# Kernel tuning notes

Measured on AMD Instinct MI355X. Metric: run time of the kernel, lower is better.

Reference implementation:

```python
import jax, jax.numpy as jnp
import numpy as np

B, E, H, W = 32, 512, 16, 16
NH, HD = 8, 64          # num_heads = embed_dim // num_heads_channels, head_dim = 64
OUT = 512
S = H * W + 1           # spacial_dim**2 + 1 = 257 (mean token prepended)


def setup_inputs() -> dict:
    key = jax.random.key(0)
    ks = jax.random.split(key, 10)
    sc = 1.0 / np.sqrt(E).astype(np.float32)
    n = lambda k, sh, s=1.0: jax.random.normal(k, sh, jnp.float32) * s
    return {
        "x_real": n(ks[0], (B, E, H, W)),
        "x_imag": n(ks[1], (B, E, H, W)),
        # positional_embedding = (randn/sqrt(E)).to(complex64) -> imag part is zero
        "pos_r": n(ks[2], (E, S), sc),
        "pos_i": jnp.zeros((E, S), jnp.float32),
        # complex in-projection (packed q,k,v) and out-projection of the MHA
        "w_in_r": n(ks[3], (3 * E, E), sc),
        "w_in_i": n(ks[4], (3 * E, E), sc),
        "b_in_r": jnp.zeros((3 * E,), jnp.float32),
        "b_in_i": jnp.zeros((3 * E,), jnp.float32),
        "w_out_r": n(ks[5], (E, E), sc),
        "w_out_i": n(ks[6], (E, E), sc),
        "b_out_r": jnp.zeros((E,), jnp.float32),
        "b_out_i": jnp.zeros((E,), jnp.float32),
        # complex 1x1 conv projection == complex linear over channels
        "w_p_r": n(ks[7], (OUT, E), sc),
        "w_p_i": n(ks[8], (OUT, E), sc),
        "b_p_r": jnp.zeros((OUT,), jnp.float32),
        "b_p_i": jnp.zeros((OUT,), jnp.float32),
    }


def _attention_pool(x_real, x_imag, pos_r, pos_i, w_in_r, w_in_i, b_in_r, b_in_i,
                    w_out_r, w_out_i, b_out_r, b_out_i, w_p_r, w_p_i, b_p_r, b_p_i):
    cx = jax.lax.complex
    x = cx(x_real, x_imag).reshape(B, E, -1)                       # [b,c,HW]
    x = jnp.concatenate([x.mean(-1, keepdims=True), x], axis=-1)   # [b,c,S]
    x = x + cx(pos_r, pos_i)[None]                                 # + pos embed
    x = x.transpose(0, 2, 1)                                       # [b,S,E]

    qkv = jnp.einsum('bse,fe->bsf', x, cx(w_in_r, w_in_i)) + cx(b_in_r, b_in_i)
    q, k, v = jnp.split(qkv, 3, axis=-1)
    q = q.reshape(B, S, NH, HD) / jnp.sqrt(jnp.float32(HD))
    k = k.reshape(B, S, NH, HD)
    v = v.reshape(B, S, NH, HD)

    logits = jnp.einsum('bqhd,bkhd->bhqk', q, k)                   # complex scores
    # complex softmax handled separately on real/imag parts
    w = cx(jax.nn.softmax(logits.real, axis=-1),
           jax.nn.softmax(logits.imag, axis=-1))
    attn = jnp.einsum('bhqk,bkhd->bqhd', w, v).reshape(B, S, E)
    attn = jnp.einsum('bse,fe->bsf', attn, cx(w_out_r, w_out_i)) + cx(b_out_r, b_out_i)

    y = attn.transpose(0, 2, 1)                                    # [b,E,S]
    y = jnp.einsum('oc,bcs->bos', cx(w_p_r, w_p_i), y) + cx(b_p_r, b_p_i)[None, :, None]
    return y[:, :, 0]                                              # [b,OUT] complex64


def reference(x_real, x_imag, pos_r, pos_i, w_in_r, w_in_i, b_in_r, b_in_i,
              w_out_r, w_out_i, b_out_r, b_out_i, w_p_r, w_p_i, b_p_r, b_p_i):
    return _attention_pool(x_real, x_imag, pos_r, pos_i, w_in_r, w_in_i, b_in_r,
                           b_in_i, w_out_r, w_out_i, b_out_r, b_out_i,
                           w_p_r, w_p_i, b_p_r, b_p_i)
```

## Files before the change

### kernel.cpp

```cpp
#include <hip/hip_runtime.h>

#define B_  32
#define E_  512
#define HW_ 256
#define S_  257
#define NH_ 8
#define HD_ 64
#define EC_ 32
#define NCH_ (E_ / EC_)

__device__ __forceinline__ float wave_reduce(float v) {
  #pragma unroll
  for (int o = 32; o > 0; o >>= 1) v += __shfl_down(v, o, 64);
  return v;
}

__global__ void k_mean(const float* __restrict__ xr, const float* __restrict__ xi,
                       const float* __restrict__ pos_r, const float* __restrict__ pos_i,
                       float* __restrict__ mr, float* __restrict__ mi) {
  int wid  = (blockIdx.x * blockDim.x + threadIdx.x) >> 6;
  int lane = threadIdx.x & 63;
  int e = wid & (E_ - 1);
  const float* pr = xr + (size_t)wid * HW_;
  const float* pi = xi + (size_t)wid * HW_;
  float sr = 0.f, si = 0.f;
  #pragma unroll
  for (int j = 0; j < HW_; j += 64) { sr += pr[j + lane]; si += pi[j + lane]; }
  sr = wave_reduce(sr); si = wave_reduce(si);
  if (lane == 0) {
    mr[wid] = sr * (1.f / HW_) + pos_r[(size_t)e * S_];
    mi[wid] = si * (1.f / HW_) + pos_i[(size_t)e * S_];
  }
}

__global__ void k_q0(const float* __restrict__ mr, const float* __restrict__ mi,
                     const float* __restrict__ w_in_r, const float* __restrict__ w_in_i,
                     const float* __restrict__ b_in_r, const float* __restrict__ b_in_i,
                     float* __restrict__ q0r, float* __restrict__ q0i) {
  int wid  = (blockIdx.x * blockDim.x + threadIdx.x) >> 6;
  int lane = threadIdx.x & 63;
  int b = wid >> 9, f = wid & (E_ - 1);
  const float* wr = w_in_r + (size_t)f * E_;
  const float* wi = w_in_i + (size_t)f * E_;
  float ar = 0.f, ai = 0.f;
  #pragma unroll
  for (int e = lane; e < E_; e += 64) {
    float Xr = mr[b * E_ + e];
    float Xi = mi[b * E_ + e];
    float Cr = wr[e], Ci = wi[e];
    ar += Xr * Cr - Xi * Ci;
    ai += Xr * Ci + Xi * Cr;
  }
  ar = wave_reduce(ar); ai = wave_reduce(ai);
  if (lane == 0) {
    q0r[wid] = (ar + b_in_r[f]) * 0.125f;
    q0i[wid] = (ai + b_in_i[f]) * 0.125f;
  }
}

__global__ void k_u(const float* __restrict__ q0r, const float* __restrict__ q0i,
                    const float* __restrict__ w_in_r, const float* __restrict__ w_in_i,
                    float* __restrict__ ur, float* __restrict__ ui) {
  int bh = blockIdx.x;
  int b = bh >> 3, h = bh & 7;
  int e = threadIdx.x;
  __shared__ float qr[HD_], qi[HD_];
  if (threadIdx.x < HD_) {
    qr[threadIdx.x] = q0r[b * E_ + h * HD_ + threadIdx.x];
    qi[threadIdx.x] = q0i[b * E_ + h * HD_ + threadIdx.x];
  }
  __syncthreads();
  float ar = 0.f, ai = 0.f;
  #pragma unroll 8
  for (int d = 0; d < HD_; ++d) {
    float Wr = w_in_r[(size_t)(E_ + h * HD_ + d) * E_ + e];
    float Wi = w_in_i[(size_t)(E_ + h * HD_ + d) * E_ + e];
    ar += qr[d] * Wr - qi[d] * Wi;
    ai += qr[d] * Wi + qi[d] * Wr;
  }
  ur[(size_t)bh * E_ + e] = ar;
  ui[(size_t)bh * E_ + e] = ai;
}

__global__ __launch_bounds__(256) void k_logits(
    const float* __restrict__ xr, const float* __restrict__ xi,
    const float* __restrict__ pos_r, const float* __restrict__ pos_i,
    const float* __restrict__ ur, const float* __restrict__ ui,
    float* __restrict__ part) {
  int blk = blockIdx.x;
  int b = blk / NCH_, c = blk % NCH_;
  int t = threadIdx.x;
  int e0 = c * EC_;
  __shared__ float us[EC_][NH_][2];
  { int e = t >> 3, h = t & 7;
    us[e][h][0] = ur[(size_t)(b * NH_ + h) * E_ + e0 + e];
    us[e][h][1] = ui[(size_t)(b * NH_ + h) * E_ + e0 + e]; }
  __syncthreads();
  float ar[NH_], ai[NH_];
  #pragma unroll
  for (int h = 0; h < NH_; ++h) { ar[h] = 0.f; ai[h] = 0.f; }
  const float* xrb = xr + ((size_t)b * E_ + e0) * HW_;
  const float* xib = xi + ((size_t)b * E_ + e0) * HW_;
  #pragma unroll 2
  for (int e = 0; e < EC_; ++e) {
    float Xr = xrb[e * HW_ + t] + pos_r[(size_t)(e0 + e) * S_ + t + 1];
    float Xi = xib[e * HW_ + t] + pos_i[(size_t)(e0 + e) * S_ + t + 1];
    #pragma unroll
    for (int h = 0; h < NH_; ++h) {
      float Ur = us[e][h][0], Ui = us[e][h][1];
      ar[h] += Xr * Ur - Xi * Ui;
      ai[h] += Xr * Ui + Xi * Ur;
    }
  }
  float2* p2 = (float2*)part;
  #pragma unroll
  for (int h = 0; h < NH_; ++h) {
    float2 v; v.x = ar[h]; v.y = ai[h];
    p2[((size_t)(b * NH_ + h) * NCH_ + c) * 256 + t] = v;
  }
}

__device__ void softmax257(float* l, float* red, int t) {
  float v = l[t];
  float v256 = l[256];
  red[t] = v; __syncthreads();
  #pragma unroll
  for (int s = 128; s > 0; s >>= 1) { if (t < s) red[t] = fmaxf(red[t], red[t + s]); __syncthreads(); }
  float M = fmaxf(red[0], v256);
  __syncthreads();
  float ex = expf(v - M);
  float e256 = expf(v256 - M);
  red[t] = ex; __syncthreads();
  #pragma unroll
  for (int s = 128; s > 0; s >>= 1) { if (t < s) red[t] += red[t + s]; __syncthreads(); }
  float inv = 1.f / (red[0] + e256);
  __syncthreads();
  l[t] = ex * inv;
  if (t == 0) l[256] = e256 * inv;
  __syncthreads();
}

__global__ __launch_bounds__(256) void k_softmax(
    const float* __restrict__ part,
    const float* __restrict__ mr, const float* __restrict__ mi,
    const float* __restrict__ ur, const float* __restrict__ ui,
    float* __restrict__ w2) {
  int bh = blockIdx.x; int b = bh >> 3;
  int t = threadIdx.x;
  __shared__ float lr[S_], li[S_], red[256];
  const float2* p2 = (const float2*)part + (size_t)bh * NCH_ * 256;
  float sr = 0.f, si = 0.f;
  #pragma unroll
  for (int c = 0; c < NCH_; ++c) { float2 v = p2[c * 256 + t]; sr += v.x; si += v.y; }
  lr[t + 1] = sr; li[t + 1] = si;
  const float* urb = ur + (size_t)bh * E_;
  const float* uib = ui + (size_t)bh * E_;
  float p0r = 0.f, p0i = 0.f;
  #pragma unroll
  for (int e = t; e < E_; e += 256) {
    float Xr = mr[b * E_ + e];
    float Xi = mi[b * E_ + e];
    p0r += Xr * urb[e] - Xi * uib[e];
    p0i += Xr * uib[e] + Xi * urb[e];
  }
  red[t] = p0r; __syncthreads();
  #pragma unroll
  for (int s = 128; s > 0; s >>= 1) { if (t < s) red[t] += red[t + s]; __syncthreads(); }
  if (t == 0) lr[0] = red[0];
  __syncthreads();
  red[t] = p0i; __syncthreads();
  #pragma unroll
  for (int s = 128; s > 0; s >>= 1) { if (t < s) red[t] += red[t + s]; __syncthreads(); }
  if (t == 0) li[0] = red[0];
  __syncthreads();
  softmax257(lr, red, t);
  softmax257(li, red, t);
  float2* o = (float2*)w2 + (size_t)bh * S_;
  float2 v; v.x = lr[t]; v.y = li[t]; o[t] = v;
  if (t == 0) { float2 v2; v2.x = lr[256]; v2.y = li[256]; o[256] = v2; }
}

__global__ __launch_bounds__(256) void k_z(
    const float* __restrict__ xr, const float* __restrict__ xi,
    const float* __restrict__ pos_r, const float* __restrict__ pos_i,
    const float* __restrict__ mr, const float* __restrict__ mi,
    const float* __restrict__ w2,
    float* __restrict__ zr_, float* __restrict__ zi_) {
  __shared__ float2 wls[NH_ * S_];
  int t = threadIdx.x, l = t & 63, w = t >> 6;
  int b = blockIdx.x >> 6;
  int g = blockIdx.x & 63;
  const float2* w2b = (const float2*)w2 + (size_t)b * NH_ * S_;
  for (int i = t; i < NH_ * S_; i += 256) wls[i] = w2b[i];
  __syncthreads();
  #pragma unroll
  for (int r = 0; r < 2; ++r) {
    int e = g * 8 + w * 2 + r;
    const float* xre = xr + ((size_t)b * E_ + e) * HW_;
    const float* xie = xi + ((size_t)b * E_ + e) * HW_;
    const float* pre = pos_r + (size_t)e * S_;
    const float* pie = pos_i + (size_t)e * S_;
    float ar[NH_], ai[NH_];
    #pragma unroll
    for (int h = 0; h < NH_; ++h) { ar[h] = 0.f; ai[h] = 0.f; }
    #pragma unroll
    for (int j = 0; j < 4; ++j) {
      int k = 1 + l + 64 * j;
      float Xr = xre[k - 1] + pre[k];
      float Xi = xie[k - 1] + pie[k];
      #pragma unroll
      for (int h = 0; h < NH_; ++h) {
        float2 W = wls[h * S_ + k];
        ar[h] += W.x * Xr - W.y * Xi;
        ai[h] += W.x * Xi + W.y * Xr;
      }
    }
    #pragma unroll
    for (int h = 0; h < NH_; ++h) { ar[h] = wave_reduce(ar[h]); ai[h] = wave_reduce(ai[h]); }
    if (l == 0) {
      float X0r = mr[b * E_ + e];
      float X0i = mi[b * E_ + e];
      #pragma unroll
      for (int h = 0; h < NH_; ++h) {
        float2 W0 = wls[h * S_];
        zr_[(size_t)(b * NH_ + h) * E_ + e] = ar[h] + W0.x * X0r - W0.y * X0i;
        zi_[(size_t)(b * NH_ + h) * E_ + e] = ai[h] + W0.x * X0i + W0.y * X0r;
      }
    }
  }
}

__global__ void k_v(const float* __restrict__ zr, const float* __restrict__ zi,
                    const float* __restrict__ w_in_r, const float* __restrict__ w_in_i,
                    const float* __restrict__ b_in_r, const float* __restrict__ b_in_i,
                    float* __restrict__ a0r, float* __restrict__ a0i) {
  int wid  = (blockIdx.x * blockDim.x + threadIdx.x) >> 6;
  int lane = threadIdx.x & 63;
  int b = wid >> 9, f = wid & (E_ - 1);
  int h = f >> 6;
  const float* wr  = w_in_r + (size_t)(2 * E_ + f) * E_;
  const float* wi  = w_in_i + (size_t)(2 * E_ + f) * E_;
  const float* zrp = zr + (size_t)(b * NH_ + h) * E_;
  const float* zip = zi + (size_t)(b * NH_ + h) * E_;
  float ar = 0.f, ai = 0.f;
  #pragma unroll
  for (int e = lane; e < E_; e += 64) {
    float Zr = zrp[e], Zi = zip[e], Cr = wr[e], Ci = wi[e];
    ar += Zr * Cr - Zi * Ci;
    ai += Zr * Ci + Zi * Cr;
  }
  ar = wave_reduce(ar); ai = wave_reduce(ai);
  if (lane == 0) {
    float bvr = b_in_r[2 * E_ + f], bvi = b_in_i[2 * E_ + f];
    a0r[wid] = ar + (bvr - bvi);
    a0i[wid] = ai + (bvr + bvi);
  }
}

__global__ void k_mv(const float* __restrict__ inr, const float* __restrict__ ini,
                     const float* __restrict__ wr_, const float* __restrict__ wi_,
                     const float* __restrict__ br_, const float* __restrict__ bi_,
                     float* __restrict__ outr, float* __restrict__ outi) {
  int wid  = (blockIdx.x * blockDim.x + threadIdx.x) >> 6;
  int lane = threadIdx.x & 63;
  int b = wid >> 9, f = wid & (E_ - 1);
  const float* wr = wr_ + (size_t)f * E_;
  const float* wi = wi_ + (size_t)f * E_;
  const float* ir = inr + (size_t)b * E_;
  const float* ii = ini + (size_t)b * E_;
  float ar = 0.f, ai = 0.f;
  #pragma unroll
  for (int e = lane; e < E_; e += 64) {
    float Xr = ir[e], Xi = ii[e], Cr = wr[e], Ci = wi[e];
    ar += Xr * Cr - Xi * Ci;
    ai += Xr * Ci + Xi * Cr;
  }
  ar = wave_reduce(ar); ai = wave_reduce(ai);
  if (lane == 0) { outr[wid] = ar + br_[f]; outi[wid] = ai + bi_[f]; }
}

__global__ void k_final(const float* __restrict__ inr, const float* __restrict__ ini,
                        const float* __restrict__ wr_, const float* __restrict__ wi_,
                        const float* __restrict__ br_, const float* __restrict__ bi_,
                        float* __restrict__ out, int interleaved) {
  int wid  = (blockIdx.x * blockDim.x + threadIdx.x) >> 6;
  int lane = threadIdx.x & 63;
  int b = wid >> 9, f = wid & (E_ - 1);
  const float* wr = wr_ + (size_t)f * E_;
  const float* wi = wi_ + (size_t)f * E_;
  const float* ir = inr + (size_t)b * E_;
  const float* ii = ini + (size_t)b * E_;
  float ar = 0.f, ai = 0.f;
  #pragma unroll
  for (int e = lane; e < E_; e += 64) {
    float Xr = ir[e], Xi = ii[e], Cr = wr[e], Ci = wi[e];
    ar += Xr * Cr - Xi * Ci;
    ai += Xr * Ci + Xi * Cr;
  }
  ar = wave_reduce(ar); ai = wave_reduce(ai);
  if (lane == 0) {
    float rr = ar + br_[f];
    float im = ai + bi_[f];
    if (interleaved) { out[(size_t)wid * 2] = rr; out[(size_t)wid * 2 + 1] = im; }
    else             { out[wid] = rr; }
  }
}

extern "C" void kernel_launch(void* const* d_in, const int* in_sizes, int n_in,
                              void* d_out, int out_size, void* d_ws, size_t ws_size,
                              hipStream_t stream) {
  (void)in_sizes; (void)n_in; (void)ws_size;
  const float* xr      = (const float*)d_in[0];
  const float* xi      = (const float*)d_in[1];
  const float* pos_r   = (const float*)d_in[2];
  const float* pos_i   = (const float*)d_in[3];
  const float* w_in_r  = (const float*)d_in[4];
  const float* w_in_i  = (const float*)d_in[5];
  const float* b_in_r  = (const float*)d_in[6];
  const float* b_in_i  = (const float*)d_in[7];
  const float* w_out_r = (const float*)d_in[8];
  const float* w_out_i = (const float*)d_in[9];
  const float* b_out_r = (const float*)d_in[10];
  const float* b_out_i = (const float*)d_in[11];
  const float* w_p_r   = (const float*)d_in[12];
  const float* w_p_i   = (const float*)d_in[13];
  const float* b_p_r   = (const float*)d_in[14];
  const float* b_p_i   = (const float*)d_in[15];

  const int BE = B_ * E_, BHE = B_ * NH_ * E_;
  float* ws   = (float*)d_ws;
  float* mr   = ws;
  float* mi   = mr  + BE;
  float* q0r  = mi  + BE;
  float* q0i  = q0r + BE;
  float* ur   = q0i + BE;
  float* ui   = ur  + BHE;
  float* part = ui  + BHE;
  float* w2   = part + (size_t)B_ * NH_ * NCH_ * 512;
  float* zr   = w2  + (size_t)2 * B_ * NH_ * S_;
  float* zi   = zr  + BHE;
  float* a0r  = zi  + BHE;
  float* a0i  = a0r + BE;
  float* aor  = a0i + BE;
  float* aoi  = aor + BE;

  k_mean   <<<B_ * E_ / 4,  256, 0, stream>>>(xr, xi, pos_r, pos_i, mr, mi);
  k_q0     <<<B_ * E_ / 4,  256, 0, stream>>>(mr, mi, w_in_r, w_in_i, b_in_r, b_in_i, q0r, q0i);
  k_u      <<<B_ * NH_,     512, 0, stream>>>(q0r, q0i, w_in_r, w_in_i, ur, ui);
  k_logits <<<B_ * NCH_,    256, 0, stream>>>(xr, xi, pos_r, pos_i, ur, ui, part);
  k_softmax<<<B_ * NH_,     256, 0, stream>>>(part, mr, mi, ur, ui, w2);
  k_z      <<<B_ * 64,      256, 0, stream>>>(xr, xi, pos_r, pos_i, mr, mi, w2, zr, zi);
  k_v      <<<B_ * E_ / 4,  256, 0, stream>>>(zr, zi, w_in_r, w_in_i, b_in_r, b_in_i, a0r, a0i);
  k_mv     <<<B_ * E_ / 4,  256, 0, stream>>>(a0r, a0i, w_out_r, w_out_i, b_out_r, b_out_i, aor, aoi);
  k_final  <<<B_ * E_ / 4,  256, 0, stream>>>(aor, aoi, w_p_r, w_p_i, b_p_r, b_p_i,
                                              (float*)d_out, out_size >= 2 * B_ * E_);
}
```

Baseline: 190.2 us.

## Fuse q0 and u kernels, vectorize matvec loads, halve logits channel chunk

```diff
diff --git a/kernel.cpp b/kernel.cpp
--- a/kernel.cpp
+++ b/kernel.cpp
@@ -6,7 +6,7 @@
 #define S_  257
 #define NH_ 8
 #define HD_ 64
-#define EC_ 32
+#define EC_ 16
 #define NCH_ (E_ / EC_)
 
 __device__ __forceinline__ float wave_reduce(float v) {
@@ -21,11 +21,11 @@
   int wid  = (blockIdx.x * blockDim.x + threadIdx.x) >> 6;
   int lane = threadIdx.x & 63;
   int e = wid & (E_ - 1);
-  const float* pr = xr + (size_t)wid * HW_;
-  const float* pi = xi + (size_t)wid * HW_;
-  float sr = 0.f, si = 0.f;
-  #pragma unroll
-  for (int j = 0; j < HW_; j += 64) { sr += pr[j + lane]; si += pi[j + lane]; }
+  const float4* pr = (const float4*)(xr + (size_t)wid * HW_);
+  const float4* pi = (const float4*)(xi + (size_t)wid * HW_);
+  float4 a = pr[lane], c = pi[lane];
+  float sr = (a.x + a.y) + (a.z + a.w);
+  float si = (c.x + c.y) + (c.z + c.w);
   sr = wave_reduce(sr); si = wave_reduce(si);
   if (lane == 0) {
     mr[wid] = sr * (1.f / HW_) + pos_r[(size_t)e * S_];
@@ -33,53 +33,69 @@
   }
 }
 
-__global__ void k_q0(const float* __restrict__ mr, const float* __restrict__ mi,
-                     const float* __restrict__ w_in_r, const float* __restrict__ w_in_i,
-                     const float* __restrict__ b_in_r, const float* __restrict__ b_in_i,
-                     float* __restrict__ q0r, float* __restrict__ q0i) {
-  int wid  = (blockIdx.x * blockDim.x + threadIdx.x) >> 6;
-  int lane = threadIdx.x & 63;
-  int b = wid >> 9, f = wid & (E_ - 1);
-  const float* wr = w_in_r + (size_t)f * E_;
-  const float* wi = w_in_i + (size_t)f * E_;
-  float ar = 0.f, ai = 0.f;
-  #pragma unroll
-  for (int e = lane; e < E_; e += 64) {
-    float Xr = mr[b * E_ + e];
-    float Xi = mi[b * E_ + e];
-    float Cr = wr[e], Ci = wi[e];
-    ar += Xr * Cr - Xi * Ci;
-    ai += Xr * Ci + Xi * Cr;
-  }
-  ar = wave_reduce(ar); ai = wave_reduce(ai);
-  if (lane == 0) {
-    q0r[wid] = (ar + b_in_r[f]) * 0.125f;
-    q0i[wid] = (ai + b_in_i[f]) * 0.125f;
-  }
-}
-
-__global__ void k_u(const float* __restrict__ q0r, const float* __restrict__ q0i,
-                    const float* __restrict__ w_in_r, const float* __restrict__ w_in_i,
-                    float* __restrict__ ur, float* __restrict__ ui) {
-  int bh = blockIdx.x;
-  int b = bh >> 3, h = bh & 7;
-  int e = threadIdx.x;
-  __shared__ float qr[HD_], qi[HD_];
-  if (threadIdx.x < HD_) {
-    qr[threadIdx.x] = q0r[b * E_ + h * HD_ + threadIdx.x];
-    qi[threadIdx.x] = q0i[b * E_ + h * HD_ + threadIdx.x];
-  }
-  __syncthreads();
-  float ar = 0.f, ai = 0.f;
-  #pragma unroll 8
-  for (int d = 0; d < HD_; ++d) {
-    float Wr = w_in_r[(size_t)(E_ + h * HD_ + d) * E_ + e];
-    float Wi = w_in_i[(size_t)(E_ + h * HD_ + d) * E_ + e];
-    ar += qr[d] * Wr - qi[d] * Wi;
-    ai += qr[d] * Wi + qi[d] * Wr;
-  }
-  ur[(size_t)bh * E_ + e] = ar;
-  ui[(size_t)bh * E_ + e] = ai;
+__global__ __launch_bounds__(512) void k_q0u(
+    const float* __restrict__ mr, const float* __restrict__ mi,
+    const float* __restrict__ w_in_r, const float* __restrict__ w_in_i,
+    const float* __restrict__ b_in_r, const float* __restrict__ b_in_i,
+    float* __restrict__ ur, float* __restrict__ ui) {
+  int bh = blockIdx.x; int b = bh >> 3, h = bh & 7;
+  int t = threadIdx.x;
+  __shared__ float m_r[E_], m_i[E_];
+  __shared__ float p_r[HD_][9], p_i[HD_][9];
+  __shared__ float q_r[HD_], q_i[HD_];
+  {
+    const float4* mr4 = (const float4*)(mr + (size_t)b * E_);
+    const float4* mi4 = (const float4*)(mi + (size_t)b * E_);
+    if (t < 128)      ((float4*)m_r)[t]       = mr4[t];
+    else if (t < 256) ((float4*)m_i)[t - 128] = mi4[t - 128];
+  }
+  __syncthreads();
+  {
+    int fl = t >> 3, sub = t & 7;
+    int f = h * HD_ + fl;
+    const float4* wr4 = (const float4*)(w_in_r + (size_t)f * E_);
+    const float4* wi4 = (const float4*)(w_in_i + (size_t)f * E_);
+    const float4* xr4 = (const float4*)m_r;
+    const float4* xi4 = (const float4*)m_i;
+    float ar = 0.f, ai = 0.f;
+    #pragma unroll
+    for (int j = 0; j < 16; ++j) {
+      float4 Wr = wr4[sub * 16 + j], Wi = wi4[sub * 16 + j];
+      float4 Xr = xr4[sub * 16 + j], Xi = xi4[sub * 16 + j];
+      ar += Xr.x * Wr.x - Xi.x * Wi.x;  ai += Xr.x * Wi.x + Xi.x * Wr.x;
+      ar += Xr.y * Wr.y - Xi.y * Wi.y;  ai += Xr.y * Wi.y + Xi.y * Wr.y;
+      ar += Xr.z * Wr.z - Xi.z * Wi.z;  ai += Xr.z * Wi.z + Xi.z * Wr.z;
+      ar += Xr.w * Wr.w - Xi.w * Wi.w;  ai += Xr.w * Wi.w + Xi.w * Wr.w;
+    }
+    p_r[fl][sub] = ar; p_i[fl][sub] = ai;
+  }
+  __syncthreads();
+  if (t < HD_) {
+    float s = 0.f;
+    #pragma unroll
+    for (int j = 0; j < 8; ++j) s += p_r[t][j];
+    q_r[t] = (s + b_in_r[h * HD_ + t]) * 0.125f;
+  } else if (t < 2 * HD_) {
+    int d = t - HD_;
+    float s = 0.f;
+    #pragma unroll
+    for (int j = 0; j < 8; ++j) s += p_i[d][j];
+    q_i[d] = (s + b_in_i[h * HD_ + d]) * 0.125f;
+  }
+  __syncthreads();
+  {
+    int e = t;
+    float ar = 0.f, ai = 0.f;
+    #pragma unroll 8
+    for (int d = 0; d < HD_; ++d) {
+      float Wr = w_in_r[(size_t)(E_ + h * HD_ + d) * E_ + e];
+      float Wi = w_in_i[(size_t)(E_ + h * HD_ + d) * E_ + e];
+      ar += q_r[d] * Wr - q_i[d] * Wi;
+      ai += q_r[d] * Wi + q_i[d] * Wr;
+    }
+    ur[(size_t)bh * E_ + e] = ar;
+    ui[(size_t)bh * E_ + e] = ai;
+  }
 }
 
 __global__ __launch_bounds__(256) void k_logits(
@@ -88,13 +104,15 @@
     const float* __restrict__ ur, const float* __restrict__ ui,
     float* __restrict__ part) {
   int blk = blockIdx.x;
-  int b = blk / NCH_, c = blk % NCH_;
+  int b = blk >> 5, c = blk & 31;
   int t = threadIdx.x;
   int e0 = c * EC_;
   __shared__ float us[EC_][NH_][2];
-  { int e = t >> 3, h = t & 7;
+  if (t < EC_ * NH_) {
+    int e = t >> 3, h = t & 7;
     us[e][h][0] = ur[(size_t)(b * NH_ + h) * E_ + e0 + e];
-    us[e][h][1] = ui[(size_t)(b * NH_ + h) * E_ + e0 + e]; }
+    us[e][h][1] = ui[(size_t)(b * NH_ + h) * E_ + e0 + e];
+  }
   __syncthreads();
   float ar[NH_], ai[NH_];
   #pragma unroll
@@ -150,7 +168,7 @@
   __shared__ float lr[S_], li[S_], red[256];
   const float2* p2 = (const float2*)part + (size_t)bh * NCH_ * 256;
   float sr = 0.f, si = 0.f;
-  #pragma unroll
+  #pragma unroll 8
   for (int c = 0; c < NCH_; ++c) { float2 v = p2[c * 256 + t]; sr += v.x; si += v.y; }
   lr[t + 1] = sr; li[t + 1] = si;
   const float* urb = ur + (size_t)bh * E_;
@@ -238,16 +256,19 @@
   int lane = threadIdx.x & 63;
   int b = wid >> 9, f = wid & (E_ - 1);
   int h = f >> 6;
-  const float* wr  = w_in_r + (size_t)(2 * E_ + f) * E_;
-  const float* wi  = w_in_i + (size_t)(2 * E_ + f) * E_;
-  const float* zrp = zr + (size_t)(b * NH_ + h) * E_;
-  const float* zip = zi + (size_t)(b * NH_ + h) * E_;
+  const float4* wr4 = (const float4*)(w_in_r + (size_t)(2 * E_ + f) * E_);
+  const float4* wi4 = (const float4*)(w_in_i + (size_t)(2 * E_ + f) * E_);
+  const float4* zr4 = (const float4*)(zr + (size_t)(b * NH_ + h) * E_);
+  const float4* zi4 = (const float4*)(zi + (size_t)(b * NH_ + h) * E_);
   float ar = 0.f, ai = 0.f;
   #pragma unroll
-  for (int e = lane; e < E_; e += 64) {
-    float Zr = zrp[e], Zi = zip[e], Cr = wr[e], Ci = wi[e];
-    ar += Zr * Cr - Zi * Ci;
-    ai += Zr * Ci + Zi * Cr;
+  for (int j = 0; j < 2; ++j) {
+    int idx = lane * 2 + j;
+    float4 Zr = zr4[idx], Zi = zi4[idx], Wr = wr4[idx], Wi = wi4[idx];
+    ar += Zr.x * Wr.x - Zi.x * Wi.x;  ai += Zr.x * Wi.x + Zi.x * Wr.x;
+    ar += Zr.y * Wr.y - Zi.y * Wi.y;  ai += Zr.y * Wi.y + Zi.y * Wr.y;
+    ar += Zr.z * Wr.z - Zi.z * Wi.z;  ai += Zr.z * Wi.z + Zi.z * Wr.z;
+    ar += Zr.w * Wr.w - Zi.w * Wi.w;  ai += Zr.w * Wi.w + Zi.w * Wr.w;
   }
   ar = wave_reduce(ar); ai = wave_reduce(ai);
   if (lane == 0) {
@@ -264,16 +285,19 @@
   int wid  = (blockIdx.x * blockDim.x + threadIdx.x) >> 6;
   int lane = threadIdx.x & 63;
   int b = wid >> 9, f = wid & (E_ - 1);
-  const float* wr = wr_ + (size_t)f * E_;
-  const float* wi = wi_ + (size_t)f * E_;
-  const float* ir = inr + (size_t)b * E_;
-  const float* ii = ini + (size_t)b * E_;
+  const float4* wr4 = (const float4*)(wr_ + (size_t)f * E_);
+  const float4* wi4 = (const float4*)(wi_ + (size_t)f * E_);
+  const float4* ir4 = (const float4*)(inr + (size_t)b * E_);
+  const float4* ii4 = (const float4*)(ini + (size_t)b * E_);
   float ar = 0.f, ai = 0.f;
   #pragma unroll
-  for (int e = lane; e < E_; e += 64) {
-    float Xr = ir[e], Xi = ii[e], Cr = wr[e], Ci = wi[e];
-    ar += Xr * Cr - Xi * Ci;
-    ai += Xr * Ci + Xi * Cr;
+  for (int j = 0; j < 2; ++j) {
+    int idx = lane * 2 + j;
+    float4 Xr = ir4[idx], Xi = ii4[idx], Wr = wr4[idx], Wi = wi4[idx];
+    ar += Xr.x * Wr.x - Xi.x * Wi.x;  ai += Xr.x * Wi.x + Xi.x * Wr.x;
+    ar += Xr.y * Wr.y - Xi.y * Wi.y;  ai += Xr.y * Wi.y + Xi.y * Wr.y;
+    ar += Xr.z * Wr.z - Xi.z * Wi.z;  ai += Xr.z * Wi.z + Xi.z * Wr.z;
+    ar += Xr.w * Wr.w - Xi.w * Wi.w;  ai += Xr.w * Wi.w + Xi.w * Wr.w;
   }
   ar = wave_reduce(ar); ai = wave_reduce(ai);
   if (lane == 0) { outr[wid] = ar + br_[f]; outi[wid] = ai + bi_[f]; }
@@ -286,16 +310,19 @@
   int wid  = (blockIdx.x * blockDim.x + threadIdx.x) >> 6;
   int lane = threadIdx.x & 63;
   int b = wid >> 9, f = wid & (E_ - 1);
-  const float* wr = wr_ + (size_t)f * E_;
-  const float* wi = wi_ + (size_t)f * E_;
-  const float* ir = inr + (size_t)b * E_;
-  const float* ii = ini + (size_t)b * E_;
+  const float4* wr4 = (const float4*)(wr_ + (size_t)f * E_);
+  const float4* wi4 = (const float4*)(wi_ + (size_t)f * E_);
+  const float4* ir4 = (const float4*)(inr + (size_t)b * E_);
+  const float4* ii4 = (const float4*)(ini + (size_t)b * E_);
   float ar = 0.f, ai = 0.f;
   #pragma unroll
-  for (int e = lane; e < E_; e += 64) {
-    float Xr = ir[e], Xi = ii[e], Cr = wr[e], Ci = wi[e];
-    ar += Xr * Cr - Xi * Ci;
-    ai += Xr * Ci + Xi * Cr;
+  for (int j = 0; j < 2; ++j) {
+    int idx = lane * 2 + j;
+    float4 Xr = ir4[idx], Xi = ii4[idx], Wr = wr4[idx], Wi = wi4[idx];
+    ar += Xr.x * Wr.x - Xi.x * Wi.x;  ai += Xr.x * Wi.x + Xi.x * Wr.x;
+    ar += Xr.y * Wr.y - Xi.y * Wi.y;  ai += Xr.y * Wi.y + Xi.y * Wr.y;
+    ar += Xr.z * Wr.z - Xi.z * Wi.z;  ai += Xr.z * Wi.z + Xi.z * Wr.z;
+    ar += Xr.w * Wr.w - Xi.w * Wi.w;  ai += Xr.w * Wi.w + Xi.w * Wr.w;
   }
   ar = wave_reduce(ar); ai = wave_reduce(ai);
   if (lane == 0) {
@@ -331,9 +358,7 @@
   float* ws   = (float*)d_ws;
   float* mr   = ws;
   float* mi   = mr  + BE;
-  float* q0r  = mi  + BE;
-  float* q0i  = q0r + BE;
-  float* ur   = q0i + BE;
+  float* ur   = mi  + BE;
   float* ui   = ur  + BHE;
   float* part = ui  + BHE;
   float* w2   = part + (size_t)B_ * NH_ * NCH_ * 512;
@@ -345,8 +370,7 @@
   float* aoi  = aor + BE;
 
   k_mean   <<<B_ * E_ / 4,  256, 0, stream>>>(xr, xi, pos_r, pos_i, mr, mi);
-  k_q0     <<<B_ * E_ / 4,  256, 0, stream>>>(mr, mi, w_in_r, w_in_i, b_in_r, b_in_i, q0r, q0i);
-  k_u      <<<B_ * NH_,     512, 0, stream>>>(q0r, q0i, w_in_r, w_in_i, ur, ui);
+  k_q0u    <<<B_ * NH_,     512, 0, stream>>>(mr, mi, w_in_r, w_in_i, b_in_r, b_in_i, ur, ui);
   k_logits <<<B_ * NCH_,    256, 0, stream>>>(xr, xi, pos_r, pos_i, ur, ui, part);
   k_softmax<<<B_ * NH_,     256, 0, stream>>>(part, mr, mi, ur, ui, w2);
   k_z      <<<B_ * 64,      256, 0, stream>>>(xr, xi, pos_r, pos_i, mr, mi, w2, zr, zi);
```

Result: slower. 195.3 us (+2.7%).
